# Optimization experiments

Hardware: AMD Instinct MI355X
Metric: run time of the kernel (lower is better)

The kernel has to match this reference:

```python
import jax, jax.numpy as jnp
import numpy as np

N = 40000      # nodes
E = 640000     # edges
R = 4          # relations (n_edge_features)
F = 128        # n_node_features
H = 128        # n_hidden
NB = 2         # num_convolution_blocks
G = 64         # graphs in batch
OUT = 10       # n_output
MAXDEG = 10    # PyG MFConv default max_degree


def setup_inputs() -> dict:
    key = jax.random.key(0)
    ks = jax.random.split(key, 20)
    s = 0.05
    return {
        "x": jax.random.normal(ks[0], (N, F), dtype=jnp.float32),
        "edge_index": jax.random.randint(ks[1], (2, E), 0, N, dtype=jnp.int32),
        "edge_attr": jax.random.randint(ks[2], (E,), 0, R, dtype=jnp.int32),
        "batch_idx": jnp.sort(jax.random.randint(ks[3], (N,), 0, G, dtype=jnp.int32)),
        # node embedding Linear(F -> H)
        "W0": jax.random.normal(ks[4], (F, H), dtype=jnp.float32) * s,
        "b0": jnp.zeros((H,), dtype=jnp.float32),
        # per-block RGCNConv params (stacked over blocks)
        "rgcn_Wrel": jax.random.normal(ks[5], (NB, R, H, H), dtype=jnp.float32) * s,
        "rgcn_Wroot": jax.random.normal(ks[6], (NB, H, H), dtype=jnp.float32) * s,
        "rgcn_b": jnp.zeros((NB, H), dtype=jnp.float32),
        # per-block MFConv params: lins_l (bias) and lins_r (no bias), one per degree 0..MAXDEG
        "mf_Wl": jax.random.normal(ks[7], (NB, MAXDEG + 1, H, H), dtype=jnp.float32) * s,
        "mf_bl": jnp.zeros((NB, MAXDEG + 1, H), dtype=jnp.float32),
        "mf_Wr": jax.random.normal(ks[8], (NB, MAXDEG + 1, H, H), dtype=jnp.float32) * s,
        # after-pool MLP
        "W1": jax.random.normal(ks[9], (H, H), dtype=jnp.float32) * s,
        "b1": jnp.zeros((H,), dtype=jnp.float32),
        "W2": jax.random.normal(ks[10], (H, OUT), dtype=jnp.float32) * s,
        "b2": jnp.zeros((OUT,), dtype=jnp.float32),
    }


def _rgcn(h, Wrel, Wroot, b, src, dst, etype):
    # PyG RGCNConv: per-relation mean of neighbor features, then relation GEMM, plus root + bias
    n = h.shape[0]
    idx = dst * R + etype                                   # fused (node, relation) segment id
    msg = h[src]                                            # [E, H] gather
    sums = jax.ops.segment_sum(msg, idx, num_segments=n * R).reshape(n, R, -1)
    cnt = jax.ops.segment_sum(jnp.ones((msg.shape[0],), h.dtype), idx,
                              num_segments=n * R).reshape(n, R, 1)
    mean = jnp.where(cnt > 0, sums / jnp.maximum(cnt, 1.0), 0.0)
    return jnp.einsum('nrh,rho->no', mean, Wrel) + h @ Wroot + b


def _mfconv(h, Wl, bl, Wr, src, dst, deg):
    # PyG MFConv: sum-aggregate neighbors, then degree-specific lin_l(agg) + lin_r(x)
    n = h.shape[0]
    agg = jax.ops.segment_sum(h[src], dst, num_segments=n)  # [N, H]
    out = jnp.zeros((n, Wl.shape[-1]), h.dtype)
    for d in range(MAXDEG + 1):                             # small fixed loop over degree buckets
        m = (deg == d).astype(h.dtype)[:, None]
        out = out + m * (agg @ Wl[d] + bl[d] + h @ Wr[d])
    return out


def reference(x, edge_index, edge_attr, batch_idx,
              W0, b0, rgcn_Wrel, rgcn_Wroot, rgcn_b,
              mf_Wl, mf_bl, mf_Wr, W1, b1, W2, b2):
    src, dst = edge_index[0], edge_index[1]
    etype = edge_attr
    n = x.shape[0]
    # node degree at targets (all relations), clamped to MAXDEG (PyG MFConv)
    deg = jnp.clip(jax.ops.segment_sum(jnp.ones((src.shape[0],), jnp.int32), dst,
                                       num_segments=n), 0, MAXDEG)
    h = x @ W0 + b0
    for blk in range(NB):
        h = jax.nn.relu(h)
        h = _rgcn(h, rgcn_Wrel[blk], rgcn_Wroot[blk], rgcn_b[blk], src, dst, etype)
        h = jax.nn.relu(h)
        h = _mfconv(h, mf_Wl[blk], mf_bl[blk], mf_Wr[blk], src, dst, deg)
    pooled = jax.ops.segment_sum(h, batch_idx, num_segments=G)  # global add pool [G, H]
    out = jax.nn.relu(pooled @ W1 + b1) @ W2 + b2
    return out
```

## Files before the change

kernel.cpp:

```cpp
#include <hip/hip_runtime.h>
#include <hip/hip_bf16.h>

#define N_NODES 40000
#define N_EDGES 640000
#define R_REL 4
#define F_IN 128
#define H_DIM 128
#define NBLK 2
#define G_GRAPHS 64
#define N_OUT 10
#define MAXDEG 10
#define NSCAN_BLK ((N_NODES + 255) / 256)

typedef unsigned short u16;
typedef float f32x4 __attribute__((ext_vector_type(4)));
typedef short bf16x8 __attribute__((ext_vector_type(8)));

__device__ __forceinline__ float relu_f(float x){ return x > 0.f ? x : 0.f; }

__device__ __forceinline__ u16 f2bf(float f){
  union { float f; unsigned int u; } v; v.f = f;
  unsigned int r = v.u + 0x7fffu + ((v.u >> 16) & 1u);
  return (u16)(r >> 16);
}
__device__ __forceinline__ float b2f(u16 u){
  union { unsigned int u; float f; } v; v.u = ((unsigned int)u) << 16; return v.f;
}
__device__ __forceinline__ float blo(unsigned v){ return b2f((u16)v); }
__device__ __forceinline__ float bhi(unsigned v){ return b2f((u16)(v >> 16)); }

__device__ __forceinline__ void gload16(const void* g, void* l){
  __builtin_amdgcn_global_load_lds(
      (const __attribute__((address_space(1))) void*)g,
      (__attribute__((address_space(3))) void*)l, 16, 0, 0);
}

__global__ void k_cnt(const int* __restrict__ dst, const int* __restrict__ et, int* __restrict__ cnt4){
  int e = blockIdx.x * blockDim.x + threadIdx.x;
  if (e >= N_EDGES) return;
  atomicAdd(&cnt4[dst[e] * R_REL + et[e]], 1);
}

__global__ __launch_bounds__(256) void k_scan_a(const int* __restrict__ cnt4, int* __restrict__ deg,
                                                int* __restrict__ row_ptr, int* __restrict__ bsum,
                                                int* __restrict__ bhist){
  __shared__ int s[256];
  __shared__ int lh[16];
  int tid = threadIdx.x;
  int i = blockIdx.x * 256 + tid;
  if (tid < 16) lh[tid] = 0;
  int d = 0;
  if (i < N_NODES){
    int4 c = *(const int4*)(cnt4 + (size_t)i * 4);
    d = c.x + c.y + c.z + c.w;
    deg[i] = d;
  }
  s[tid] = d;
  __syncthreads();
  if (i < N_NODES){
    int dc = d > MAXDEG ? MAXDEG : d;
    atomicAdd(&lh[dc], 1);
  }
  for (int o = 1; o < 256; o <<= 1){
    int t = (tid >= o) ? s[tid - o] : 0;
    __syncthreads();
    s[tid] += t;
    __syncthreads();
  }
  if (i < N_NODES) row_ptr[i] = s[tid] - d;
  if (tid == 255) bsum[blockIdx.x] = s[255];
  if (tid <= MAXDEG) bhist[blockIdx.x * (MAXDEG + 1) + tid] = lh[tid];
}

__global__ __launch_bounds__(256) void k_scan_b(int* __restrict__ bsum, int* __restrict__ bbase){
  __shared__ int s[256];
  int tid = threadIdx.x;
  int v = (tid < NSCAN_BLK) ? bsum[tid] : 0;
  s[tid] = v;
  __syncthreads();
  for (int o = 1; o < 256; o <<= 1){
    int t = (tid >= o) ? s[tid - o] : 0;
    __syncthreads();
    s[tid] += t;
    __syncthreads();
  }
  if (tid < NSCAN_BLK) bbase[tid] = s[tid] - v;
}

__global__ __launch_bounds__(256) void k_scan_c(int* __restrict__ row_ptr, const int* __restrict__ bbase,
                                                const int* __restrict__ cnt4, int* __restrict__ rel_off){
  int i = blockIdx.x * 256 + threadIdx.x;
  if (i < N_NODES){
    int base = row_ptr[i] + bbase[blockIdx.x];
    row_ptr[i] = base;
    int4 c = *(const int4*)(cnt4 + (size_t)i * 4);
    int4 o;
    o.x = base;
    o.y = base + c.x;
    o.z = o.y + c.y;
    o.w = o.z + c.z;
    *(int4*)(rel_off + (size_t)i * 4) = o;
  }
  if (i == 0) row_ptr[N_NODES] = N_EDGES;
}

__global__ void k_csr_fill(const int* __restrict__ src, const int* __restrict__ dst,
                           const int* __restrict__ et, const int* __restrict__ rel_off,
                           int* __restrict__ cursor, int* __restrict__ esrc){
  int e = blockIdx.x * blockDim.x + threadIdx.x;
  if (e >= N_EDGES) return;
  int cell = dst[e] * R_REL + et[e];
  int p = atomicAdd(&cursor[cell], 1);
  esrc[rel_off[cell] + p] = src[e];
}

__global__ __launch_bounds__(64) void k_bscan(const int* __restrict__ bhist, int* __restrict__ pbase,
                                              int* __restrict__ bcount, int* __restrict__ boff){
  __shared__ int cnt_s[MAXDEG + 1];
  __shared__ int off_s[MAXDEG + 1];
  int d = threadIdx.x;
  if (d <= MAXDEG){
    int run = 0;
    for (int b = 0; b < NSCAN_BLK; ++b){
      pbase[b * (MAXDEG + 1) + d] = run;
      run += bhist[b * (MAXDEG + 1) + d];
    }
    cnt_s[d] = run;
    bcount[d] = run;
  }
  __syncthreads();
  if (d == 0){
    int s = 0;
    for (int dd = 0; dd <= MAXDEG; ++dd){ off_s[dd] = s; boff[dd] = s; s += cnt_s[dd]; }
  }
  __syncthreads();
  if (d <= MAXDEG){
    int base = off_s[d];
    for (int b = 0; b < NSCAN_BLK; ++b) pbase[b * (MAXDEG + 1) + d] += base;
  }
}

__global__ __launch_bounds__(256) void k_bfill(const int* __restrict__ deg, const int* __restrict__ pbase,
                                               int* __restrict__ perm){
  __shared__ int lh[MAXDEG + 1];
  int tid = threadIdx.x;
  if (tid <= MAXDEG) lh[tid] = 0;
  __syncthreads();
  int i = blockIdx.x * 256 + tid;
  if (i < N_NODES){
    int d = deg[i]; if (d > MAXDEG) d = MAXDEG;
    int lpos = atomicAdd(&lh[d], 1);
    perm[pbase[blockIdx.x * (MAXDEG + 1) + d] + lpos] = i;
  }
}

__global__ __launch_bounds__(256) void k_cvtW_all(const float* __restrict__ s0, const float* __restrict__ s1,
                                                  const float* __restrict__ s2, const float* __restrict__ s3,
                                                  const float* __restrict__ s4,
                                                  u16* __restrict__ d0, u16* __restrict__ d1,
                                                  u16* __restrict__ d2, u16* __restrict__ d3,
                                                  u16* __restrict__ d4){
  __shared__ float s[32][33];
  int b = blockIdx.x;
  int m = b >> 4, tile = b & 15;
  const float* S; u16* D; int base;
  if (m < 1){ S = s0; D = d0; base = m; }
  else if (m < 9){ S = s1; D = d1; base = m - 1; }
  else if (m < 11){ S = s2; D = d2; base = m - 9; }
  else if (m < 33){ S = s3; D = d3; base = m - 11; }
  else { S = s4; D = d4; base = m - 33; }
  S += (size_t)base * 16384;
  D += (size_t)base * 16384;
  int tr = (tile >> 2) * 32, tc = (tile & 3) * 32;
  int c = threadIdx.x & 31, r0 = threadIdx.x >> 5;
  #pragma unroll
  for (int i = 0; i < 4; ++i){
    int r = r0 + i * 8;
    s[r][c] = S[(size_t)(tr + r) * 128 + tc + c];
  }
  __syncthreads();
  #pragma unroll
  for (int i = 0; i < 4; ++i){
    int r = r0 + i * 8;
    D[(size_t)(tc + r) * 128 + tr + c] = f2bf(s[c][r]);
  }
}

__global__ void k_cvtx(const float* __restrict__ x, u16* __restrict__ xb){
  int t = blockIdx.x * 256 + threadIdx.x;
  if (t >= (N_NODES * H_DIM) / 4) return;
  float4 v = ((const float4*)x)[t];
  uint2 o = make_uint2((unsigned)f2bf(v.x) | ((unsigned)f2bf(v.y) << 16),
                       (unsigned)f2bf(v.z) | ((unsigned)f2bf(v.w) << 16));
  ((uint2*)xb)[t] = o;
}

__global__ __launch_bounds__(256) void k_rgcn_agg(const u16* __restrict__ hb,
                                                  const int* __restrict__ rel_off,
                                                  const int* __restrict__ row_ptr,
                                                  const int* __restrict__ esrc,
                                                  u16* __restrict__ meanb){
  int node = blockIdx.x * 4 + (threadIdx.x >> 6);
  int lane = threadIdx.x & 63;
  int4 ro = *(const int4*)(rel_off + (size_t)node * 4);
  int nend = row_ptr[node + 1];
  int begs[5] = {ro.x, ro.y, ro.z, ro.w, nend};
  #pragma unroll
  for (int r = 0; r < R_REL; ++r){
    int beg = begs[r], end = begs[r + 1];
    float a0 = 0.f, a1 = 0.f;
    int e = beg;
    for (; e + 4 <= end; e += 4){
      int s0 = esrc[e], s1 = esrc[e + 1], s2 = esrc[e + 2], s3 = esrc[e + 3];
      unsigned v0 = *(const unsigned*)(hb + (size_t)s0 * H_DIM + lane * 2);
      unsigned v1 = *(const unsigned*)(hb + (size_t)s1 * H_DIM + lane * 2);
      unsigned v2 = *(const unsigned*)(hb + (size_t)s2 * H_DIM + lane * 2);
      unsigned v3 = *(const unsigned*)(hb + (size_t)s3 * H_DIM + lane * 2);
      a0 += blo(v0) + blo(v1) + blo(v2) + blo(v3);
      a1 += bhi(v0) + bhi(v1) + bhi(v2) + bhi(v3);
    }
    for (; e < end; ++e){
      unsigned v = *(const unsigned*)(hb + (size_t)esrc[e] * H_DIM + lane * 2);
      a0 += blo(v); a1 += bhi(v);
    }
    int c = end - beg;
    float inv = c > 0 ? 1.f / (float)c : 0.f;
    unsigned o = (unsigned)f2bf(a0 * inv) | ((unsigned)f2bf(a1 * inv) << 16);
    *(unsigned*)(meanb + ((size_t)node * R_REL + r) * H_DIM + lane * 2) = o;
  }
}

__global__ __launch_bounds__(256) void k_mf_agg(const u16* __restrict__ hb,
                                                const int* __restrict__ row_ptr,
                                                const int* __restrict__ esrc,
                                                u16* __restrict__ aggb){
  int node = blockIdx.x * 4 + (threadIdx.x >> 6);
  int lane = threadIdx.x & 63;
  int beg = row_ptr[node], end = row_ptr[node + 1];
  float a0 = 0.f, a1 = 0.f;
  int e = beg;
  for (; e + 4 <= end; e += 4){
    int s0 = esrc[e], s1 = esrc[e + 1], s2 = esrc[e + 2], s3 = esrc[e + 3];
    unsigned v0 = *(const unsigned*)(hb + (size_t)s0 * H_DIM + lane * 2);
    unsigned v1 = *(const unsigned*)(hb + (size_t)s1 * H_DIM + lane * 2);
    unsigned v2 = *(const unsigned*)(hb + (size_t)s2 * H_DIM + lane * 2);
    unsigned v3 = *(const unsigned*)(hb + (size_t)s3 * H_DIM + lane * 2);
    a0 += blo(v0) + blo(v1) + blo(v2) + blo(v3);
    a1 += bhi(v0) + bhi(v1) + bhi(v2) + bhi(v3);
  }
  for (; e < end; ++e){
    unsigned v = *(const unsigned*)(hb + (size_t)esrc[e] * H_DIM + lane * 2);
    a0 += blo(v); a1 += bhi(v);
  }
  unsigned o = (unsigned)f2bf(a0) | ((unsigned)f2bf(a1) << 16);
  *(unsigned*)(aggb + (size_t)node * H_DIM + lane * 2) = o;
}


__global__ __launch_bounds__(512) void k_gemm0(const u16* __restrict__ xb, const u16* __restrict__ wt,
                                               const float* __restrict__ bias, u16* __restrict__ hbo){
  __shared__ u16 lds[32][128];
  int tid = threadIdx.x;
  int w = tid >> 6, lane = tid & 63;
  int m0 = blockIdx.x * 32;
  int rg = lane >> 4, cb = (lane & 15) << 4;
  int srow = w * 4 + rg;
  int swcb = cb ^ ((srow & 7) << 4);
  gload16(xb + (size_t)(m0 + srow) * F_IN + (swcb >> 1), &lds[w * 4][0]);
  __syncthreads();

  int arow = lane & 15, kg = lane >> 4;
  int col = w * 16 + arow;
  f32x4 acc[2];
  acc[0] = (f32x4){0.f, 0.f, 0.f, 0.f};
  acc[1] = (f32x4){0.f, 0.f, 0.f, 0.f};
  bf16x8 b[4];
  #pragma unroll
  for (int kk = 0; kk < 4; ++kk)
    b[kk] = *(const bf16x8*)(wt + (size_t)col * F_IN + kk * 32 + kg * 8);
  #pragma unroll
  for (int rt = 0; rt < 2; ++rt){
    int row = rt * 16 + arow;
    const char* base = (const char*)&lds[0][0] + row * 256;
    int sx = (row & 7) << 4;
    #pragma unroll
    for (int kk = 0; kk < 4; ++kk){
      bf16x8 a = *(const bf16x8*)(base + ((kk * 64 + kg * 16) ^ sx));
      acc[rt] = __builtin_amdgcn_mfma_f32_16x16x32_bf16(a, b[kk], acc[rt], 0, 0, 0);
    }
  }
  float bb = bias[col];
  #pragma unroll
  for (int rt = 0; rt < 2; ++rt)
    #pragma unroll
    for (int j = 0; j < 4; ++j){
      int gr = m0 + rt * 16 + kg * 4 + j;
      hbo[(size_t)gr * H_DIM + col] = f2bf(relu_f(acc[rt][j] + bb));
    }
}

__global__ __launch_bounds__(512) void k_rgcn_gemm(const u16* __restrict__ meanb, const u16* __restrict__ hb,
                                                   const u16* __restrict__ wrel, const u16* __restrict__ wroot,
                                                   const float* __restrict__ bias, u16* __restrict__ hbo){
  __shared__ u16 lds[5][32][128];
  int tid = threadIdx.x;
  int w = tid >> 6, lane = tid & 63;
  int m0 = blockIdx.x * 32;
  int rg = lane >> 4, cb = (lane & 15) << 4;
  int srow = w * 4 + rg;
  int swcb = cb ^ ((srow & 7) << 4);
  #pragma unroll
  for (int s = 0; s < 4; ++s)
    gload16(meanb + ((size_t)(m0 + srow) * R_REL + s) * H_DIM + (swcb >> 1), &lds[s][w * 4][0]);
  gload16(hb + (size_t)(m0 + srow) * H_DIM + (swcb >> 1), &lds[4][w * 4][0]);
  __syncthreads();

  int arow = lane & 15, kg = lane >> 4;
  int col = w * 16 + arow;
  f32x4 acc[2];
  acc[0] = (f32x4){0.f, 0.f, 0.f, 0.f};
  acc[1] = (f32x4){0.f, 0.f, 0.f, 0.f};
  #pragma unroll
  for (int s = 0; s < 5; ++s){
    const u16* WT = (s < 4) ? wrel + (size_t)s * 16384 : wroot;
    bf16x8 b[4];
    #pragma unroll
    for (int kk = 0; kk < 4; ++kk)
      b[kk] = *(const bf16x8*)(WT + (size_t)col * H_DIM + kk * 32 + kg * 8);
    #pragma unroll
    for (int rt = 0; rt < 2; ++rt){
      int row = rt * 16 + arow;
      const char* base = (const char*)&lds[s][0][0] + row * 256;
      int sx = (row & 7) << 4;
      #pragma unroll
      for (int kk = 0; kk < 4; ++kk){
        bf16x8 a = *(const bf16x8*)(base + ((kk * 64 + kg * 16) ^ sx));
        acc[rt] = __builtin_amdgcn_mfma_f32_16x16x32_bf16(a, b[kk], acc[rt], 0, 0, 0);
      }
    }
  }
  float bb = bias[col];
  #pragma unroll
  for (int rt = 0; rt < 2; ++rt)
    #pragma unroll
    for (int j = 0; j < 4; ++j){
      int gr = m0 + rt * 16 + kg * 4 + j;
      hbo[(size_t)gr * H_DIM + col] = f2bf(relu_f(acc[rt][j] + bb));
    }
}

template<int FINAL>
__global__ __launch_bounds__(512) void k_mf_gemm(const u16* __restrict__ aggb, const u16* __restrict__ hb,
                                                 const u16* __restrict__ wl, const u16* __restrict__ wr,
                                                 const float* __restrict__ bl,
                                                 const int* __restrict__ bcount, const int* __restrict__ boff,
                                                 const int* __restrict__ perm,
                                                 u16* __restrict__ hbo, float* __restrict__ hf){
  __shared__ u16 lds[2][32][128];
  __shared__ int rows_s[32];
  int t = blockIdx.x;
  int d = -1, tile = 0;
  for (int dd = 0; dd <= MAXDEG; ++dd){
    int nt = (bcount[dd] + 31) >> 5;
    if (t < nt){ d = dd; tile = t; break; }
    t -= nt;
  }
  if (d < 0) return;
  int cnt_d = bcount[d];
  int start = boff[d] + tile * 32;
  int nrows = cnt_d - tile * 32; if (nrows > 32) nrows = 32;

  int tid = threadIdx.x;
  int w = tid >> 6, lane = tid & 63;
  if (tid < 32) rows_s[tid] = (tid < nrows) ? perm[start + tid] : -1;

  int rg = lane >> 4, cb = (lane & 15) << 4;
  int srow = w * 4 + rg;
  int swcb = cb ^ ((srow & 7) << 4);
  int node = perm[start + (srow < nrows ? srow : 0)];
  gload16(aggb + (size_t)node * H_DIM + (swcb >> 1), &lds[0][w * 4][0]);
  gload16(hb   + (size_t)node * H_DIM + (swcb >> 1), &lds[1][w * 4][0]);
  __syncthreads();

  int arow = lane & 15, kg = lane >> 4;
  int col = w * 16 + arow;
  f32x4 acc[2];
  acc[0] = (f32x4){0.f, 0.f, 0.f, 0.f};
  acc[1] = (f32x4){0.f, 0.f, 0.f, 0.f};
  #pragma unroll
  for (int s = 0; s < 2; ++s){
    const u16* WT = (s ? wr : wl) + (size_t)d * 16384;
    bf16x8 b[4];
    #pragma unroll
    for (int kk = 0; kk < 4; ++kk)
      b[kk] = *(const bf16x8*)(WT + (size_t)col * H_DIM + kk * 32 + kg * 8);
    #pragma unroll
    for (int rt = 0; rt < 2; ++rt){
      int row = rt * 16 + arow;
      const char* base = (const char*)&lds[s][0][0] + row * 256;
      int sx = (row & 7) << 4;
      #pragma unroll
      for (int kk = 0; kk < 4; ++kk){
        bf16x8 a = *(const bf16x8*)(base + ((kk * 64 + kg * 16) ^ sx));
        acc[rt] = __builtin_amdgcn_mfma_f32_16x16x32_bf16(a, b[kk], acc[rt], 0, 0, 0);
      }
    }
  }
  float bb = bl[(size_t)d * H_DIM + col];
  #pragma unroll
  for (int rt = 0; rt < 2; ++rt)
    #pragma unroll
    for (int j = 0; j < 4; ++j){
      int gr = rows_s[rt * 16 + kg * 4 + j];
      if (gr >= 0){
        float v = acc[rt][j] + bb;
        if (FINAL) hf[(size_t)gr * H_DIM + col] = v;
        else       hbo[(size_t)gr * H_DIM + col] = f2bf(relu_f(v));
      }
    }
}

__global__ void k_goff(const int* __restrict__ batch, int* __restrict__ goff){
  int n = blockIdx.x * blockDim.x + threadIdx.x;
  if (n >= N_NODES) return;
  int b = batch[n];
  int bp = (n == 0) ? -1 : batch[n - 1];
  for (int g = bp + 1; g <= b; ++g) goff[g] = n;
  if (n == N_NODES - 1){
    for (int g = b + 1; g <= G_GRAPHS; ++g) goff[g] = N_NODES;
  }
}

__global__ __launch_bounds__(256) void k_pool(const float* __restrict__ h, const int* __restrict__ goff,
                                              float* __restrict__ pooled){
  __shared__ float4 sred[8][32];
  int g = blockIdx.x;
  int tid = threadIdx.x;
  int rg = tid >> 5, lane = tid & 31;
  int beg = goff[g], end = goff[g + 1];
  float4 acc = make_float4(0.f, 0.f, 0.f, 0.f);
  for (int n = beg + rg; n < end; n += 8){
    float4 v = ((const float4*)(h + (size_t)n * H_DIM))[lane];
    acc.x += v.x; acc.y += v.y; acc.z += v.z; acc.w += v.w;
  }
  sred[rg][lane] = acc;
  __syncthreads();
  if (tid < 32){
    float4 s = sred[0][tid];
    #pragma unroll
    for (int r = 1; r < 8; ++r){
      float4 v = sred[r][tid];
      s.x += v.x; s.y += v.y; s.z += v.z; s.w += v.w;
    }
    *(float4*)(pooled + (size_t)g * H_DIM + tid * 4) = s;
  }
}

__global__ void k_mlp1(const float* __restrict__ pooled, const float* __restrict__ W1,
                       const float* __restrict__ b1, float* __restrict__ T){
  int t = blockIdx.x * blockDim.x + threadIdx.x;
  if (t >= G_GRAPHS * H_DIM) return;
  int n = t >> 7, j = t & 127;
  float s = b1[j];
  for (int k = 0; k < H_DIM; ++k) s += pooled[n * H_DIM + k] * W1[k * H_DIM + j];
  T[t] = relu_f(s);
}

__global__ void k_mlp2(const float* __restrict__ T, const float* __restrict__ W2,
                       const float* __restrict__ b2, float* __restrict__ out){
  int t = blockIdx.x * blockDim.x + threadIdx.x;
  if (t >= G_GRAPHS * N_OUT) return;
  int n = t / N_OUT, j = t - n * N_OUT;
  float s = b2[j];
  for (int k = 0; k < H_DIM; ++k) s += T[n * H_DIM + k] * W2[k * N_OUT + j];
  out[t] = s;
}

extern "C" void kernel_launch(void* const* d_in, const int* in_sizes, int n_in,
                              void* d_out, int out_size, void* d_ws, size_t ws_size,
                              hipStream_t stream){
  const float* x      = (const float*)d_in[0];
  const int*   ei     = (const int*)d_in[1];
  const int*   ea     = (const int*)d_in[2];
  const int*   batch  = (const int*)d_in[3];
  const float* W0     = (const float*)d_in[4];
  const float* b0     = (const float*)d_in[5];
  const float* rWrel  = (const float*)d_in[6];
  const float* rWroot = (const float*)d_in[7];
  const float* rb     = (const float*)d_in[8];
  const float* mWl    = (const float*)d_in[9];
  const float* mbl    = (const float*)d_in[10];
  const float* mWr    = (const float*)d_in[11];
  const float* W1     = (const float*)d_in[12];
  const float* b1     = (const float*)d_in[13];
  const float* W2     = (const float*)d_in[14];
  const float* b2     = (const float*)d_in[15];
  float* out = (float*)d_out;

  const int* src = ei;
  const int* dst = ei + N_EDGES;

  char* ws = (char*)d_ws;
  size_t off = 0;
  auto alloc = [&](size_t bytes) -> void* {
    void* p = ws + off;
    off += (bytes + 255) & ~(size_t)255;
    return p;
  };
  u16* xb      = (u16*)alloc((size_t)N_NODES * H_DIM * 2);
  u16* hbA     = (u16*)alloc((size_t)N_NODES * H_DIM * 2);
  u16* hbB     = (u16*)alloc((size_t)N_NODES * H_DIM * 2);
  u16* meanb   = (u16*)alloc((size_t)N_NODES * R_REL * H_DIM * 2);
  u16* aggb    = meanb;
  float* hf    = (float*)alloc((size_t)N_NODES * H_DIM * 4);
  u16* wt0     = (u16*)alloc((size_t)1 * 16384 * 2);
  u16* wtRel   = (u16*)alloc((size_t)NBLK * R_REL * 16384 * 2);
  u16* wtRoot  = (u16*)alloc((size_t)NBLK * 16384 * 2);
  u16* wtWl    = (u16*)alloc((size_t)NBLK * (MAXDEG + 1) * 16384 * 2);
  u16* wtWr    = (u16*)alloc((size_t)NBLK * (MAXDEG + 1) * 16384 * 2);
  float* pooled = (float*)alloc((size_t)G_GRAPHS * H_DIM * 4);
  float* T      = (float*)alloc((size_t)G_GRAPHS * H_DIM * 4);
  int* cnt4     = (int*)alloc((size_t)N_NODES * R_REL * 4);
  int* deg      = (int*)alloc((size_t)N_NODES * 4);
  int* row_ptr  = (int*)alloc((size_t)(N_NODES + 1) * 4);
  int* rel_off  = (int*)alloc((size_t)N_NODES * R_REL * 4);
  int* cursor   = (int*)alloc((size_t)N_NODES * R_REL * 4);
  int* esrc     = (int*)alloc((size_t)N_EDGES * 4);
  int* bsum     = (int*)alloc((size_t)NSCAN_BLK * 4);
  int* bbase    = (int*)alloc((size_t)NSCAN_BLK * 4);
  int* bhist    = (int*)alloc((size_t)NSCAN_BLK * (MAXDEG + 1) * 4);
  int* pbase    = (int*)alloc((size_t)NSCAN_BLK * (MAXDEG + 1) * 4);
  int* perm     = (int*)alloc((size_t)N_NODES * 4);
  int* bcount   = (int*)alloc(16 * 4);
  int* boff     = (int*)alloc(16 * 4);
  int* goff     = (int*)alloc((size_t)(G_GRAPHS + 1) * 4);

  hipMemsetAsync(cnt4, 0, (size_t)N_NODES * R_REL * 4, stream);
  hipMemsetAsync(cursor, 0, (size_t)N_NODES * R_REL * 4, stream);

  k_cnt<<<(N_EDGES + 255) / 256, 256, 0, stream>>>(dst, ea, cnt4);
  k_scan_a<<<NSCAN_BLK, 256, 0, stream>>>(cnt4, deg, row_ptr, bsum, bhist);
  k_scan_b<<<1, 256, 0, stream>>>(bsum, bbase);
  k_scan_c<<<NSCAN_BLK, 256, 0, stream>>>(row_ptr, bbase, cnt4, rel_off);
  k_csr_fill<<<(N_EDGES + 255) / 256, 256, 0, stream>>>(src, dst, ea, rel_off, cursor, esrc);
  k_bscan<<<1, 64, 0, stream>>>(bhist, pbase, bcount, boff);
  k_bfill<<<NSCAN_BLK, 256, 0, stream>>>(deg, pbase, perm);
  k_goff<<<(N_NODES + 255) / 256, 256, 0, stream>>>(batch, goff);

  k_cvtW_all<<<55 * 16, 256, 0, stream>>>(W0, rWrel, rWroot, mWl, mWr,
                                          wt0, wtRel, wtRoot, wtWl, wtWr);
  k_cvtx<<<(N_NODES * H_DIM / 4 + 255) / 256, 256, 0, stream>>>(x, xb);

  k_gemm0<<<N_NODES / 32, 512, 0, stream>>>(xb, wt0, b0, hbA);

  u16* hin = hbA;
  u16* hout = hbB;
  for (int blk = 0; blk < NBLK; ++blk){
    k_rgcn_agg<<<N_NODES / 4, 256, 0, stream>>>(hin, rel_off, row_ptr, esrc, meanb);
    k_rgcn_gemm<<<N_NODES / 32, 512, 0, stream>>>(meanb, hin,
        wtRel + (size_t)blk * R_REL * 16384,
        wtRoot + (size_t)blk * 16384,
        rb + (size_t)blk * H_DIM, hout);
    { u16* tmp = hin; hin = hout; hout = tmp; }

    k_mf_agg<<<N_NODES / 4, 256, 0, stream>>>(hin, row_ptr, esrc, aggb);
    const u16* wl_b = wtWl + (size_t)blk * (MAXDEG + 1) * 16384;
    const u16* wr_b = wtWr + (size_t)blk * (MAXDEG + 1) * 16384;
    const float* bl_b = mbl + (size_t)blk * (MAXDEG + 1) * H_DIM;
    int grid_mf = N_NODES / 32 + MAXDEG + 1;
    if (blk == NBLK - 1)
      k_mf_gemm<1><<<grid_mf, 512, 0, stream>>>(aggb, hin, wl_b, wr_b, bl_b,
                                                bcount, boff, perm, hout, hf);
    else
      k_mf_gemm<0><<<grid_mf, 512, 0, stream>>>(aggb, hin, wl_b, wr_b, bl_b,
                                                bcount, boff, perm, hout, hf);
    { u16* tmp = hin; hin = hout; hout = tmp; }
  }

  k_pool<<<G_GRAPHS, 256, 0, stream>>>(hf, goff, pooled);
  k_mlp1<<<(G_GRAPHS * H_DIM + 255) / 256, 256, 0, stream>>>(pooled, W1, b1, T);
  k_mlp2<<<(G_GRAPHS * N_OUT + 255) / 256, 256, 0, stream>>>(T, W2, b2, out);
}
```

Measured before the change: 400.5 us.

## Fuse scan and MLP kernels, init cursor from offsets, interleave relation gathers

New measurement: 436.5 us. 1.09x slower.

```diff
diff --git a/kernel.cpp b/kernel.cpp
--- a/kernel.cpp
+++ b/kernel.cpp
@@ -72,8 +72,12 @@
   if (tid <= MAXDEG) bhist[blockIdx.x * (MAXDEG + 1) + tid] = lh[tid];
 }
 
-__global__ __launch_bounds__(256) void k_scan_b(int* __restrict__ bsum, int* __restrict__ bbase){
+__global__ __launch_bounds__(256) void k_scan_bb(int* __restrict__ bsum, int* __restrict__ bbase,
+                                                 const int* __restrict__ bhist, int* __restrict__ pbase,
+                                                 int* __restrict__ bcount, int* __restrict__ boff){
   __shared__ int s[256];
+  __shared__ int cnt_s[MAXDEG + 1];
+  __shared__ int off_s[MAXDEG + 1];
   int tid = threadIdx.x;
   int v = (tid < NSCAN_BLK) ? bsum[tid] : 0;
   s[tid] = v;
@@ -85,10 +89,31 @@
     __syncthreads();
   }
   if (tid < NSCAN_BLK) bbase[tid] = s[tid] - v;
+
+  if (tid <= MAXDEG){
+    int run = 0;
+    for (int b = 0; b < NSCAN_BLK; ++b){
+      pbase[b * (MAXDEG + 1) + tid] = run;
+      run += bhist[b * (MAXDEG + 1) + tid];
+    }
+    cnt_s[tid] = run;
+    bcount[tid] = run;
+  }
+  __syncthreads();
+  if (tid == 0){
+    int acc = 0;
+    for (int dd = 0; dd <= MAXDEG; ++dd){ off_s[dd] = acc; boff[dd] = acc; acc += cnt_s[dd]; }
+  }
+  __syncthreads();
+  if (tid <= MAXDEG){
+    int base = off_s[tid];
+    for (int b = 0; b < NSCAN_BLK; ++b) pbase[b * (MAXDEG + 1) + tid] += base;
+  }
 }
 
 __global__ __launch_bounds__(256) void k_scan_c(int* __restrict__ row_ptr, const int* __restrict__ bbase,
-                                                const int* __restrict__ cnt4, int* __restrict__ rel_off){
+                                                const int* __restrict__ cnt4, int* __restrict__ rel_off,
+                                                int* __restrict__ cursor){
   int i = blockIdx.x * 256 + threadIdx.x;
   if (i < N_NODES){
     int base = row_ptr[i] + bbase[blockIdx.x];
@@ -100,44 +125,19 @@
     o.z = o.y + c.y;
     o.w = o.z + c.z;
     *(int4*)(rel_off + (size_t)i * 4) = o;
+    *(int4*)(cursor + (size_t)i * 4) = o;
   }
   if (i == 0) row_ptr[N_NODES] = N_EDGES;
 }
 
 __global__ void k_csr_fill(const int* __restrict__ src, const int* __restrict__ dst,
-                           const int* __restrict__ et, const int* __restrict__ rel_off,
+                           const int* __restrict__ et,
                            int* __restrict__ cursor, int* __restrict__ esrc){
   int e = blockIdx.x * blockDim.x + threadIdx.x;
   if (e >= N_EDGES) return;
   int cell = dst[e] * R_REL + et[e];
   int p = atomicAdd(&cursor[cell], 1);
-  esrc[rel_off[cell] + p] = src[e];
-}
-
-__global__ __launch_bounds__(64) void k_bscan(const int* __restrict__ bhist, int* __restrict__ pbase,
-                                              int* __restrict__ bcount, int* __restrict__ boff){
-  __shared__ int cnt_s[MAXDEG + 1];
-  __shared__ int off_s[MAXDEG + 1];
-  int d = threadIdx.x;
-  if (d <= MAXDEG){
-    int run = 0;
-    for (int b = 0; b < NSCAN_BLK; ++b){
-      pbase[b * (MAXDEG + 1) + d] = run;
-      run += bhist[b * (MAXDEG + 1) + d];
-    }
-    cnt_s[d] = run;
-    bcount[d] = run;
-  }
-  __syncthreads();
-  if (d == 0){
-    int s = 0;
-    for (int dd = 0; dd <= MAXDEG; ++dd){ off_s[dd] = s; boff[dd] = s; s += cnt_s[dd]; }
-  }
-  __syncthreads();
-  if (d <= MAXDEG){
-    int base = off_s[d];
-    for (int b = 0; b < NSCAN_BLK; ++b) pbase[b * (MAXDEG + 1) + d] += base;
-  }
+  esrc[p] = src[e];
 }
 
 __global__ __launch_bounds__(256) void k_bfill(const int* __restrict__ deg, const int* __restrict__ pbase,
@@ -204,30 +204,39 @@
   int lane = threadIdx.x & 63;
   int4 ro = *(const int4*)(rel_off + (size_t)node * 4);
   int nend = row_ptr[node + 1];
-  int begs[5] = {ro.x, ro.y, ro.z, ro.w, nend};
-  #pragma unroll
-  for (int r = 0; r < R_REL; ++r){
-    int beg = begs[r], end = begs[r + 1];
-    float a0 = 0.f, a1 = 0.f;
-    int e = beg;
-    for (; e + 4 <= end; e += 4){
-      int s0 = esrc[e], s1 = esrc[e + 1], s2 = esrc[e + 2], s3 = esrc[e + 3];
-      unsigned v0 = *(const unsigned*)(hb + (size_t)s0 * H_DIM + lane * 2);
-      unsigned v1 = *(const unsigned*)(hb + (size_t)s1 * H_DIM + lane * 2);
-      unsigned v2 = *(const unsigned*)(hb + (size_t)s2 * H_DIM + lane * 2);
-      unsigned v3 = *(const unsigned*)(hb + (size_t)s3 * H_DIM + lane * 2);
-      a0 += blo(v0) + blo(v1) + blo(v2) + blo(v3);
-      a1 += bhi(v0) + bhi(v1) + bhi(v2) + bhi(v3);
-    }
-    for (; e < end; ++e){
-      unsigned v = *(const unsigned*)(hb + (size_t)esrc[e] * H_DIM + lane * 2);
-      a0 += blo(v); a1 += bhi(v);
-    }
-    int c = end - beg;
-    float inv = c > 0 ? 1.f / (float)c : 0.f;
-    unsigned o = (unsigned)f2bf(a0 * inv) | ((unsigned)f2bf(a1 * inv) << 16);
-    *(unsigned*)(meanb + ((size_t)node * R_REL + r) * H_DIM + lane * 2) = o;
-  }
+  int e0 = ro.x, e1 = ro.y, e2 = ro.z, e3 = ro.w;
+  int E0 = ro.y, E1 = ro.z, E2 = ro.w, E3 = nend;
+  int c0 = E0 - e0, c1 = E1 - e1, c2 = E2 - e2, c3 = E3 - e3;
+  float a00 = 0.f, a01 = 0.f, a10 = 0.f, a11 = 0.f;
+  float a20 = 0.f, a21 = 0.f, a30 = 0.f, a31 = 0.f;
+  const u16* hl = hb + lane * 2;
+  while ((e0 < E0) | (e1 < E1) | (e2 < E2) | (e3 < E3)){
+    if (e0 < E0){
+      unsigned v = *(const unsigned*)(hl + (size_t)esrc[e0] * H_DIM);
+      a00 += blo(v); a01 += bhi(v); ++e0;
+    }
+    if (e1 < E1){
+      unsigned v = *(const unsigned*)(hl + (size_t)esrc[e1] * H_DIM);
+      a10 += blo(v); a11 += bhi(v); ++e1;
+    }
+    if (e2 < E2){
+      unsigned v = *(const unsigned*)(hl + (size_t)esrc[e2] * H_DIM);
+      a20 += blo(v); a21 += bhi(v); ++e2;
+    }
+    if (e3 < E3){
+      unsigned v = *(const unsigned*)(hl + (size_t)esrc[e3] * H_DIM);
+      a30 += blo(v); a31 += bhi(v); ++e3;
+    }
+  }
+  float i0 = c0 > 0 ? 1.f / (float)c0 : 0.f;
+  float i1 = c1 > 0 ? 1.f / (float)c1 : 0.f;
+  float i2 = c2 > 0 ? 1.f / (float)c2 : 0.f;
+  float i3 = c3 > 0 ? 1.f / (float)c3 : 0.f;
+  unsigned* mb = (unsigned*)(meanb + (size_t)node * R_REL * H_DIM + lane * 2);
+  mb[0]                = (unsigned)f2bf(a00 * i0) | ((unsigned)f2bf(a01 * i0) << 16);
+  mb[H_DIM / 2]        = (unsigned)f2bf(a10 * i1) | ((unsigned)f2bf(a11 * i1) << 16);
+  mb[H_DIM]            = (unsigned)f2bf(a20 * i2) | ((unsigned)f2bf(a21 * i2) << 16);
+  mb[3 * H_DIM / 2]    = (unsigned)f2bf(a30 * i3) | ((unsigned)f2bf(a31 * i3) << 16);
 }
 
 __global__ __launch_bounds__(256) void k_mf_agg(const u16* __restrict__ hb,
@@ -237,21 +246,38 @@
   int node = blockIdx.x * 4 + (threadIdx.x >> 6);
   int lane = threadIdx.x & 63;
   int beg = row_ptr[node], end = row_ptr[node + 1];
-  float a0 = 0.f, a1 = 0.f;
+  const u16* hl = hb + lane * 2;
+  float a0 = 0.f, a1 = 0.f, b0 = 0.f, b1 = 0.f;
+  float c0 = 0.f, c1 = 0.f, d0 = 0.f, d1 = 0.f;
   int e = beg;
-  for (; e + 4 <= end; e += 4){
-    int s0 = esrc[e], s1 = esrc[e + 1], s2 = esrc[e + 2], s3 = esrc[e + 3];
-    unsigned v0 = *(const unsigned*)(hb + (size_t)s0 * H_DIM + lane * 2);
-    unsigned v1 = *(const unsigned*)(hb + (size_t)s1 * H_DIM + lane * 2);
-    unsigned v2 = *(const unsigned*)(hb + (size_t)s2 * H_DIM + lane * 2);
-    unsigned v3 = *(const unsigned*)(hb + (size_t)s3 * H_DIM + lane * 2);
-    a0 += blo(v0) + blo(v1) + blo(v2) + blo(v3);
-    a1 += bhi(v0) + bhi(v1) + bhi(v2) + bhi(v3);
-  }
-  for (; e < end; ++e){
-    unsigned v = *(const unsigned*)(hb + (size_t)esrc[e] * H_DIM + lane * 2);
+  for (; e + 8 <= end; e += 8){
+    int s0 = esrc[e],     s1 = esrc[e + 1], s2 = esrc[e + 2], s3 = esrc[e + 3];
+    int s4 = esrc[e + 4], s5 = esrc[e + 5], s6 = esrc[e + 6], s7 = esrc[e + 7];
+    unsigned v0 = *(const unsigned*)(hl + (size_t)s0 * H_DIM);
+    unsigned v1 = *(const unsigned*)(hl + (size_t)s1 * H_DIM);
+    unsigned v2 = *(const unsigned*)(hl + (size_t)s2 * H_DIM);
+    unsigned v3 = *(const unsigned*)(hl + (size_t)s3 * H_DIM);
+    unsigned v4 = *(const unsigned*)(hl + (size_t)s4 * H_DIM);
+    unsigned v5 = *(const unsigned*)(hl + (size_t)s5 * H_DIM);
+    unsigned v6 = *(const unsigned*)(hl + (size_t)s6 * H_DIM);
+    unsigned v7 = *(const unsigned*)(hl + (size_t)s7 * H_DIM);
+    a0 += blo(v0) + blo(v4); a1 += bhi(v0) + bhi(v4);
+    b0 += blo(v1) + blo(v5); b1 += bhi(v1) + bhi(v5);
+    c0 += blo(v2) + blo(v6); c1 += bhi(v2) + bhi(v6);
+    d0 += blo(v3) + blo(v7); d1 += bhi(v3) + bhi(v7);
+  }
+  for (; e + 2 <= end; e += 2){
+    unsigned v0 = *(const unsigned*)(hl + (size_t)esrc[e] * H_DIM);
+    unsigned v1 = *(const unsigned*)(hl + (size_t)esrc[e + 1] * H_DIM);
+    a0 += blo(v0); a1 += bhi(v0);
+    b0 += blo(v1); b1 += bhi(v1);
+  }
+  if (e < end){
+    unsigned v = *(const unsigned*)(hl + (size_t)esrc[e] * H_DIM);
     a0 += blo(v); a1 += bhi(v);
   }
+  a0 += b0 + c0 + d0;
+  a1 += b1 + c1 + d1;
   unsigned o = (unsigned)f2bf(a0) | ((unsigned)f2bf(a1) << 16);
   *(unsigned*)(aggb + (size_t)node * H_DIM + lane * 2) = o;
 }
@@ -456,24 +482,22 @@
   }
 }
 
-__global__ void k_mlp1(const float* __restrict__ pooled, const float* __restrict__ W1,
-                       const float* __restrict__ b1, float* __restrict__ T){
-  int t = blockIdx.x * blockDim.x + threadIdx.x;
-  if (t >= G_GRAPHS * H_DIM) return;
-  int n = t >> 7, j = t & 127;
+__global__ __launch_bounds__(128) void k_mlp(const float* __restrict__ pooled,
+                                             const float* __restrict__ W1, const float* __restrict__ b1,
+                                             const float* __restrict__ W2, const float* __restrict__ b2,
+                                             float* __restrict__ out){
+  __shared__ float Ts[128];
+  int g = blockIdx.x, j = threadIdx.x;
+  const float* p = pooled + (size_t)g * H_DIM;
   float s = b1[j];
-  for (int k = 0; k < H_DIM; ++k) s += pooled[n * H_DIM + k] * W1[k * H_DIM + j];
-  T[t] = relu_f(s);
-}
-
-__global__ void k_mlp2(const float* __restrict__ T, const float* __restrict__ W2,
-                       const float* __restrict__ b2, float* __restrict__ out){
-  int t = blockIdx.x * blockDim.x + threadIdx.x;
-  if (t >= G_GRAPHS * N_OUT) return;
-  int n = t / N_OUT, j = t - n * N_OUT;
-  float s = b2[j];
-  for (int k = 0; k < H_DIM; ++k) s += T[n * H_DIM + k] * W2[k * N_OUT + j];
-  out[t] = s;
+  for (int k = 0; k < H_DIM; ++k) s += p[k] * W1[k * H_DIM + j];
+  Ts[j] = relu_f(s);
+  __syncthreads();
+  if (j < N_OUT){
+    float o = b2[j];
+    for (int k = 0; k < H_DIM; ++k) o += Ts[k] * W2[k * N_OUT + j];
+    out[(size_t)g * N_OUT + j] = o;
+  }
 }
 
 extern "C" void kernel_launch(void* const* d_in, const int* in_sizes, int n_in,
@@ -519,7 +543,6 @@
   u16* wtWl    = (u16*)alloc((size_t)NBLK * (MAXDEG + 1) * 16384 * 2);
   u16* wtWr    = (u16*)alloc((size_t)NBLK * (MAXDEG + 1) * 16384 * 2);
   float* pooled = (float*)alloc((size_t)G_GRAPHS * H_DIM * 4);
-  float* T      = (float*)alloc((size_t)G_GRAPHS * H_DIM * 4);
   int* cnt4     = (int*)alloc((size_t)N_NODES * R_REL * 4);
   int* deg      = (int*)alloc((size_t)N_NODES * 4);
   int* row_ptr  = (int*)alloc((size_t)(N_NODES + 1) * 4);
@@ -536,14 +559,12 @@
   int* goff     = (int*)alloc((size_t)(G_GRAPHS + 1) * 4);
 
   hipMemsetAsync(cnt4, 0, (size_t)N_NODES * R_REL * 4, stream);
-  hipMemsetAsync(cursor, 0, (size_t)N_NODES * R_REL * 4, stream);
 
   k_cnt<<<(N_EDGES + 255) / 256, 256, 0, stream>>>(dst, ea, cnt4);
   k_scan_a<<<NSCAN_BLK, 256, 0, stream>>>(cnt4, deg, row_ptr, bsum, bhist);
-  k_scan_b<<<1, 256, 0, stream>>>(bsum, bbase);
-  k_scan_c<<<NSCAN_BLK, 256, 0, stream>>>(row_ptr, bbase, cnt4, rel_off);
-  k_csr_fill<<<(N_EDGES + 255) / 256, 256, 0, stream>>>(src, dst, ea, rel_off, cursor, esrc);
-  k_bscan<<<1, 64, 0, stream>>>(bhist, pbase, bcount, boff);
+  k_scan_bb<<<1, 256, 0, stream>>>(bsum, bbase, bhist, pbase, bcount, boff);
+  k_scan_c<<<NSCAN_BLK, 256, 0, stream>>>(row_ptr, bbase, cnt4, rel_off, cursor);
+  k_csr_fill<<<(N_EDGES + 255) / 256, 256, 0, stream>>>(src, dst, ea, cursor, esrc);
   k_bfill<<<NSCAN_BLK, 256, 0, stream>>>(deg, pbase, perm);
   k_goff<<<(N_NODES + 255) / 256, 256, 0, stream>>>(batch, goff);
 
@@ -578,6 +599,5 @@
   }
 
   k_pool<<<G_GRAPHS, 256, 0, stream>>>(hf, goff, pooled);
-  k_mlp1<<<(G_GRAPHS * H_DIM + 255) / 256, 256, 0, stream>>>(pooled, W1, b1, T);
-  k_mlp2<<<(G_GRAPHS * N_OUT + 255) / 256, 256, 0, stream>>>(T, W2, b2, out);
-}
+  k_mlp<<<G_GRAPHS, 128, 0, stream>>>(pooled, W1, b1, W2, b2, out);
+}
```
